# Kernel optimization log

Hardware: AMD Instinct MI355X
Metric: run time of the kernel (lower is better)

Reference implementation:

```python
import jax, jax.numpy as jnp
import numpy as np

# Qwen3-0.6B-like config; 4 equal-length requests flattened into [R*S, H]
L, R, S, H = 2, 4, 1024, 1024
NH, NKV, DH = 16, 8, 128
FF = 3072
EPS = 1e-6
THETA = 1e6
SCALE = 0.02  # weight init scale to keep activations sane


def setup_inputs() -> dict:
    key = jax.random.key(0)
    ks = jax.random.split(key, 8)
    return {
        "hidden_states": jax.random.normal(ks[0], (R * S, H), jnp.float32),
        "Wq": jax.random.normal(ks[1], (L, H, NH * DH), jnp.float32) * SCALE,
        "Wk": jax.random.normal(ks[2], (L, H, NKV * DH), jnp.float32) * SCALE,
        "Wv": jax.random.normal(ks[3], (L, H, NKV * DH), jnp.float32) * SCALE,
        "Wo": jax.random.normal(ks[4], (L, NH * DH, H), jnp.float32) * SCALE,
        "q_norm_w": jnp.ones((L, DH), jnp.float32),
        "k_norm_w": jnp.ones((L, DH), jnp.float32),
        "ln1_w": jnp.ones((L, H), jnp.float32),
        "ln2_w": jnp.ones((L, H), jnp.float32),
        "Wg": jax.random.normal(ks[5], (L, H, FF), jnp.float32) * SCALE,
        "Wu": jax.random.normal(ks[6], (L, H, FF), jnp.float32) * SCALE,
        "Wd": jax.random.normal(ks[7], (L, FF, H), jnp.float32) * SCALE,
        "final_norm_w": jnp.ones((H,), jnp.float32),
    }


def _rms(x, w):
    return x * jax.lax.rsqrt(jnp.mean(x * x, axis=-1, keepdims=True) + EPS) * w


def _rope_tables():
    inv_freq = 1.0 / (THETA ** (jnp.arange(0, DH, 2, dtype=jnp.float32) / DH))
    pos = jnp.arange(S, dtype=jnp.float32)  # per-request positions 0..S-1 (prefill)
    freqs = pos[:, None] * inv_freq[None, :]        # [S, DH/2]
    emb = jnp.concatenate([freqs, freqs], axis=-1)  # [S, DH]
    return jnp.cos(emb), jnp.sin(emb)


def _rotate_half(x):
    x1, x2 = jnp.split(x, 2, axis=-1)
    return jnp.concatenate([-x2, x1], axis=-1)


def _apply_rope(x, cos, sin):
    # x: [R, heads, S, DH]; cos/sin: [S, DH]
    c = cos[None, None]
    s = sin[None, None]
    return x * c + _rotate_half(x) * s


def reference(hidden_states, Wq, Wk, Wv, Wo, q_norm_w, k_norm_w, ln1_w, ln2_w,
              Wg, Wu, Wd, final_norm_w):
    cos, sin = _rope_tables()
    causal = jnp.tril(jnp.ones((S, S), dtype=bool))  # per-request causal mask
    neg = jnp.finfo(hidden_states.dtype).min
    scaling = 1.0 / jnp.sqrt(jnp.asarray(DH, hidden_states.dtype))

    x = hidden_states
    for l in range(L):
        # --- attention block ---
        residual = x
        h = _rms(x, ln1_w[l])                       # [R*S, H]
        q = (h @ Wq[l]).reshape(R, S, NH, DH)
        k = (h @ Wk[l]).reshape(R, S, NKV, DH)
        v = (h @ Wv[l]).reshape(R, S, NKV, DH)
        q = _rms(q, q_norm_w[l]).transpose(0, 2, 1, 3)   # [R, NH, S, DH]
        k = _rms(k, k_norm_w[l]).transpose(0, 2, 1, 3)   # [R, NKV, S, DH]
        v = v.transpose(0, 2, 1, 3)                      # [R, NKV, S, DH]
        q = _apply_rope(q, cos, sin)
        k = _apply_rope(k, cos, sin)
        # GQA: repeat KV heads
        rep = NH // NKV
        k = jnp.repeat(k, rep, axis=1)
        v = jnp.repeat(v, rep, axis=1)
        scores = jnp.einsum('rhqd,rhkd->rhqk', q, k) * scaling
        scores = jnp.where(causal[None, None], scores, neg)
        attn = jax.nn.softmax(scores, axis=-1)
        o = jnp.einsum('rhqk,rhkd->rhqd', attn, v)       # [R, NH, S, DH]
        o = o.transpose(0, 2, 1, 3).reshape(R * S, NH * DH)
        x = residual + o @ Wo[l]
        # --- MLP block ---
        residual = x
        h = _rms(x, ln2_w[l])
        x = residual + (jax.nn.silu(h @ Wg[l]) * (h @ Wu[l])) @ Wd[l]
    return _rms(x, final_norm_w)
```

## Files before the change

### kernel.cpp

```cpp
#include <hip/hip_runtime.h>
#include <hip/hip_bf16.h>

typedef __bf16 bf16;
typedef __bf16 bf16x8 __attribute__((ext_vector_type(8)));
typedef float f32x4 __attribute__((ext_vector_type(4)));

#define DEVINL __device__ __forceinline__

constexpr int L_ = 2, R_ = 4, S_ = 1024, H_ = 1024;
constexpr int NH_ = 16, NKV_ = 8, DH_ = 128;
constexpr int FF_ = 3072;
constexpr int T_ = R_ * S_;

DEVINL void gload16(const bf16* g, bf16* l) {
    __builtin_amdgcn_global_load_lds(
        (const __attribute__((address_space(1))) void*)g,
        (__attribute__((address_space(3))) void*)l, 16, 0, 0);
}

__global__ void rope_tables_kernel(float* __restrict__ cosb, float* __restrict__ sinb) {
    int s = blockIdx.x;
    int i = threadIdx.x;
    float inv = __expf(-(float)i * (1.0f / 64.0f) * 13.815510557964274f);
    float f = (float)s * inv;
    cosb[s * 64 + i] = cosf(f);
    sinb[s * 64 + i] = sinf(f);
}

template <bool OUT_BF16>
__global__ __launch_bounds__(256) void rmsnorm_kernel(const float* __restrict__ x,
                                                      const float* __restrict__ w,
                                                      void* __restrict__ out) {
    int row = blockIdx.x;
    const float* xr = x + (size_t)row * H_;
    int t = threadIdx.x;
    float v[4];
    float ss = 0.f;
#pragma unroll
    for (int j = 0; j < 4; ++j) {
        v[j] = xr[t + 256 * j];
        ss += v[j] * v[j];
    }
#pragma unroll
    for (int off = 32; off; off >>= 1) ss += __shfl_xor(ss, off);
    __shared__ float part[4];
    if ((t & 63) == 0) part[t >> 6] = ss;
    __syncthreads();
    ss = part[0] + part[1] + part[2] + part[3];
    float r = rsqrtf(ss * (1.0f / (float)H_) + 1e-6f);
#pragma unroll
    for (int j = 0; j < 4; ++j) {
        int c = t + 256 * j;
        float o = v[j] * r * w[c];
        if constexpr (OUT_BF16)
            ((bf16*)out)[(size_t)row * H_ + c] = (bf16)o;
        else
            ((float*)out)[(size_t)row * H_ + c] = o;
    }
}

__global__ __launch_bounds__(256) void transpose_all_kernel(
    const float* __restrict__ Wq, const float* __restrict__ Wk, const float* __restrict__ Wv,
    const float* __restrict__ Wo, const float* __restrict__ Wg, const float* __restrict__ Wu,
    const float* __restrict__ Wd, bf16* __restrict__ wqkv_t, bf16* __restrict__ wo_t,
    bf16* __restrict__ wgu_t, bf16* __restrict__ wd_t) {
    __shared__ float tile[32][33];
    int bid = blockIdx.x;
    const float* in;
    bf16* out;
    int Rk, Cn, mode, tid;
    if (bid < 2048) { in = Wq; out = wqkv_t; Rk = 1024; Cn = 2048; mode = 0; tid = bid; }
    else if (bid < 3072) { in = Wk; out = wqkv_t + (size_t)2048 * 1024; Rk = 1024; Cn = 1024; mode = 0; tid = bid - 2048; }
    else if (bid < 4096) { in = Wv; out = wqkv_t + (size_t)3072 * 1024; Rk = 1024; Cn = 1024; mode = 0; tid = bid - 3072; }
    else if (bid < 6144) { in = Wo; out = wo_t; Rk = 2048; Cn = 1024; mode = 0; tid = bid - 4096; }
    else if (bid < 9216) { in = Wg; out = wgu_t; Rk = 1024; Cn = 3072; mode = 1; tid = bid - 6144; }
    else if (bid < 12288) { in = Wu; out = wgu_t; Rk = 1024; Cn = 3072; mode = 2; tid = bid - 9216; }
    else { in = Wd; out = wd_t; Rk = 3072; Cn = 1024; mode = 0; tid = bid - 12288; }
    int nbx = Cn >> 5;
    int c0 = (tid % nbx) * 32, r0 = (tid / nbx) * 32;
    int t = threadIdx.x;
    int tc = t & 31, tr = t >> 5;
#pragma unroll
    for (int i = 0; i < 4; ++i) {
        int r = tr + i * 8;
        tile[r][tc] = in[(size_t)(r0 + r) * Cn + c0 + tc];
    }
    __syncthreads();
#pragma unroll
    for (int i = 0; i < 4; ++i) {
        int c = c0 + tr + i * 8;
        int n = (mode == 0) ? c : (((c >> 4) << 5) + ((mode == 2) ? 16 : 0) + (c & 15));
        out[(size_t)n * Rk + r0 + tc] = (bf16)tile[tc][tr + i * 8];
    }
}

__global__ __launch_bounds__(256) void vt_kernel(const bf16* __restrict__ qkv,
                                                 bf16* __restrict__ vt) {
    __shared__ bf16 tile[32][34];
    int s0 = blockIdx.x * 32, c0 = blockIdx.y * 32, r = blockIdx.z;
    int t = threadIdx.x, tc = t & 31, tr = t >> 5;
#pragma unroll
    for (int i = 0; i < 4; ++i) {
        int s = tr + i * 8;
        tile[s][tc] = qkv[(size_t)(r * 1024 + s0 + s) * 4096 + 3072 + c0 + tc];
    }
    __syncthreads();
#pragma unroll
    for (int i = 0; i < 4; ++i) {
        int c = tr + i * 8;
        vt[((size_t)(r * 1024 + c0 + c)) * 1024 + s0 + tc] = tile[tc][c];
    }
}

template <int EPI>
__global__ __launch_bounds__(512, 4) void gemmP_kernel(const bf16* __restrict__ A,
                                                       const bf16* __restrict__ Bt,
                                                       void* __restrict__ out,
                                                       int M, int N, int K) {
    __shared__ bf16 lds[36864];
    const int NT = K >> 5;
    int nbm = M >> 7, nbn = N >> 8;
    int slice = nbn >> 3;
    int id = blockIdx.x;
    int xcd = id & 7, wi = id >> 3;
    int bm = (wi / slice) << 7;
    int bn = (xcd * slice + wi % slice) << 8;
    int t = threadIdx.x, lane = t & 63, w = t >> 6;
    int wm = w >> 2, wn = w & 3;
    int hi = lane >> 4, f = lane & 15;

    int srow = t >> 2;
    int ssc = (t & 3) ^ ((srow >> 1) & 3);
    const bf16* aSrc = A + (size_t)(bm + srow) * K + (ssc << 3);
    const bf16* b0Src = Bt + (size_t)(bn + srow) * K + (ssc << 3);
    const bf16* b1Src = Bt + (size_t)(bn + 128 + srow) * K + (ssc << 3);

    f32x4 acc[4][4] = {};

    auto stage = [&](int tt, int sb) {
        gload16(aSrc + tt * 32, lds + sb * 4096 + w * 512);
        gload16(b0Src + tt * 32, lds + 12288 + sb * 8192 + w * 512);
        gload16(b1Src + tt * 32, lds + 12288 + sb * 8192 + 4096 + w * 512);
    };

    stage(0, 0);
    stage(1, 1);
    asm volatile("s_waitcnt vmcnt(3)" ::: "memory");
    __builtin_amdgcn_s_barrier();

    int cb = 0;
    for (int tau = 0; tau < NT; ++tau) {
        const bf16* aB = lds + cb * 4096;
        const bf16* bB = lds + 12288 + cb * 8192;
        if (tau + 2 < NT) stage(tau + 2, (cb == 0) ? 2 : cb - 1);
        bf16x8 af[4], bfv[4];
#pragma unroll
        for (int mf = 0; mf < 4; ++mf) {
            int row = wm * 64 + mf * 16 + f;
            af[mf] = *(const bf16x8*)(aB + row * 32 + ((hi ^ ((row >> 1) & 3)) << 3));
        }
#pragma unroll
        for (int nf = 0; nf < 4; ++nf) {
            int row = wn * 64 + nf * 16 + f;
            bfv[nf] = *(const bf16x8*)(bB + row * 32 + ((hi ^ ((row >> 1) & 3)) << 3));
        }
        __builtin_amdgcn_s_setprio(1);
#pragma unroll
        for (int mf = 0; mf < 4; ++mf)
#pragma unroll
            for (int nf = 0; nf < 4; ++nf)
                acc[mf][nf] = __builtin_amdgcn_mfma_f32_16x16x32_bf16(af[mf], bfv[nf],
                                                                      acc[mf][nf], 0, 0, 0);
        __builtin_amdgcn_s_setprio(0);
        if (tau < NT - 2)
            asm volatile("s_waitcnt vmcnt(3)" ::: "memory");
        else
            asm volatile("s_waitcnt vmcnt(0)" ::: "memory");
        __builtin_amdgcn_s_barrier();
        cb = (cb == 2) ? 0 : cb + 1;
    }

    int rb = bm + wm * 64 + hi * 4;
#pragma unroll
    for (int mf = 0; mf < 4; ++mf) {
        if constexpr (EPI == 5) {
#pragma unroll
            for (int p = 0; p < 2; ++p) {
                int col = ((bn + wn * 64) >> 1) + p * 16 + f;
#pragma unroll
                for (int g = 0; g < 4; ++g) {
                    float gv = acc[mf][2 * p][g], uv = acc[mf][2 * p + 1][g];
                    float sv = gv / (1.0f + __expf(-gv));
                    ((bf16*)out)[(size_t)(rb + mf * 16 + g) * (N / 2) + col] = (bf16)(sv * uv);
                }
            }
        } else {
            int cb2 = bn + wn * 64 + f;
#pragma unroll
            for (int nf = 0; nf < 4; ++nf)
#pragma unroll
                for (int g = 0; g < 4; ++g)
                    ((bf16*)out)[(size_t)(rb + mf * 16 + g) * N + cb2 + nf * 16] =
                        (bf16)acc[mf][nf][g];
        }
    }
}

template <int EPI>
__global__ __launch_bounds__(256, 2) void gemmD_kernel(const bf16* __restrict__ A,
                                                       const bf16* __restrict__ Bt,
                                                       void* __restrict__ out,
                                                       const float* __restrict__ res,
                                                       int M, int N, int K) {
    __shared__ bf16 lds[36864];
    const int NT = K >> 6;
    int nbm = M >> 6;
    int id = blockIdx.x;
    int xcd = id & 7, wi = id >> 3;
    int bm = (wi % nbm) << 6, bn = xcd << 7;
    int t = threadIdx.x, lane = t & 63, w = t >> 6;
    int wm = w >> 1, wn = w & 1;
    int hi = lane >> 4, f = lane & 15;

    int ar0 = t >> 3, ac0 = t & 7;
    const bf16* aS0 = A + (size_t)(bm + ar0) * K + (((ac0 ^ (ar0 & 7)) & 7) << 3);
    const bf16* aS1 = A + (size_t)(bm + 32 + ar0) * K + (((ac0 ^ ((ar0 + 32) & 7)) & 7) << 3);
    const bf16* bS[4];
#pragma unroll
    for (int j = 0; j < 4; ++j) {
        int row = j * 32 + ar0;
        bS[j] = Bt + (size_t)(bn + row) * K + (((ac0 ^ (row & 7)) & 7) << 3);
    }

    f32x4 acc[2][4] = {};

    auto stage = [&](int tt, int sb) {
        gload16(aS0 + tt * 64, lds + sb * 4096 + w * 512);
        gload16(aS1 + tt * 64, lds + sb * 4096 + 2048 + w * 512);
#pragma unroll
        for (int j = 0; j < 4; ++j)
            gload16(bS[j] + tt * 64, lds + 12288 + sb * 8192 + j * 2048 + w * 512);
    };

    stage(0, 0);
    stage(1, 1);
    asm volatile("s_waitcnt vmcnt(6)" ::: "memory");
    __builtin_amdgcn_s_barrier();

    int cb = 0;
    for (int tau = 0; tau < NT; ++tau) {
        const bf16* aB = lds + cb * 4096;
        const bf16* bB = lds + 12288 + cb * 8192;
        if (tau + 2 < NT) stage(tau + 2, (cb == 0) ? 2 : cb - 1);
        bf16x8 af[2][2], bfv[2][4];
#pragma unroll
        for (int kh = 0; kh < 2; ++kh) {
            int q = kh * 4 + hi;
#pragma unroll
            for (int mf = 0; mf < 2; ++mf) {
                int row = wm * 32 + mf * 16 + f;
                af[kh][mf] = *(const bf16x8*)(aB + row * 64 + ((q ^ (row & 7)) << 3));
            }
#pragma unroll
            for (int nf = 0; nf < 4; ++nf) {
                int row = wn * 64 + nf * 16 + f;
                bfv[kh][nf] = *(const bf16x8*)(bB + row * 64 + ((q ^ (row & 7)) << 3));
            }
        }
        __builtin_amdgcn_s_setprio(1);
#pragma unroll
        for (int kh = 0; kh < 2; ++kh)
#pragma unroll
            for (int mf = 0; mf < 2; ++mf)
#pragma unroll
                for (int nf = 0; nf < 4; ++nf)
                    acc[mf][nf] = __builtin_amdgcn_mfma_f32_16x16x32_bf16(
                        af[kh][mf], bfv[kh][nf], acc[mf][nf], 0, 0, 0);
        __builtin_amdgcn_s_setprio(0);
        if (tau < NT - 2)
            asm volatile("s_waitcnt vmcnt(6)" ::: "memory");
        else
            asm volatile("s_waitcnt vmcnt(0)" ::: "memory");
        __builtin_amdgcn_s_barrier();
        cb = (cb == 2) ? 0 : cb + 1;
    }

    int rb = bm + wm * 32 + hi * 4;
    int cb2 = bn + wn * 64 + f;
#pragma unroll
    for (int mf = 0; mf < 2; ++mf)
#pragma unroll
        for (int nf = 0; nf < 4; ++nf)
#pragma unroll
            for (int g = 0; g < 4; ++g) {
                size_t idx = (size_t)(rb + mf * 16 + g) * N + cb2 + nf * 16;
                ((float*)out)[idx] = acc[mf][nf][g] + res[idx];
            }
}

DEVINL void head_norm_rope(const bf16* __restrict__ src, const float* __restrict__ w,
                           const float* __restrict__ cosb, const float* __restrict__ sinb,
                           int s, int ln, bf16* __restrict__ dst) {
    float x0 = (float)src[ln], x1 = (float)src[ln + 32];
    float x2 = (float)src[ln + 64], x3 = (float)src[ln + 96];
    float ss = x0 * x0 + x1 * x1 + x2 * x2 + x3 * x3;
#pragma unroll
    for (int off = 16; off; off >>= 1) ss += __shfl_xor(ss, off);
    float rr = rsqrtf(ss * (1.0f / 128.0f) + 1e-6f);
    float n0 = x0 * rr * w[ln], n1 = x1 * rr * w[ln + 32];
    float n2 = x2 * rr * w[ln + 64], n3 = x3 * rr * w[ln + 96];
    float c0 = cosb[s * 64 + ln], c1 = cosb[s * 64 + ln + 32];
    float s0 = sinb[s * 64 + ln], s1 = sinb[s * 64 + ln + 32];
    dst[ln] = (bf16)(n0 * c0 - n2 * s0);
    dst[ln + 32] = (bf16)(n1 * c1 - n3 * s1);
    dst[ln + 64] = (bf16)(n2 * c0 + n0 * s0);
    dst[ln + 96] = (bf16)(n3 * c1 + n1 * s1);
}

__global__ __launch_bounds__(256) void qkv_post_kernel(const bf16* __restrict__ qkv,
                                                       const float* __restrict__ qw,
                                                       const float* __restrict__ kw,
                                                       const float* __restrict__ cosb,
                                                       const float* __restrict__ sinb,
                                                       bf16* __restrict__ qo,
                                                       bf16* __restrict__ ko) {
    int tok = blockIdx.x;
    int r = tok >> 10, s = tok & 1023;
    int t = threadIdx.x;
    int g = t >> 5;
    int ln = t & 31;
    const bf16* row = qkv + (size_t)tok * 4096;
#pragma unroll
    for (int hh = 0; hh < 2; ++hh) {
        int h = g + hh * 8;
        head_norm_rope(row + h * 128, qw, cosb, sinb, s, ln,
                       qo + ((size_t)(r * NH_ + h) * S_ + s) * 128);
    }
    head_norm_rope(row + 2048 + g * 128, kw, cosb, sinb, s, ln,
                   ko + ((size_t)(r * NKV_ + g) * S_ + s) * 128);
}

__global__ __launch_bounds__(256, 2) void flash_kernel(const bf16* __restrict__ q,
                                                       const bf16* __restrict__ k,
                                                       const bf16* __restrict__ vt,
                                                       bf16* __restrict__ out) {
    __shared__ bf16 Kl[64 * 128];
    __shared__ bf16 Vl[128 * 64];
    __shared__ bf16 Pl[4][32 * 64];
    int bid = blockIdx.x;
    int grp = bid & 63, slot = bid >> 6;
    int strip = (slot < 4) ? (7 - slot) : (slot - 4);
    int h = 2 * (grp & 7) + ((grp >> 3) & 1);
    int r = grp >> 4;
    int kvh = h >> 1;

    int t = threadIdx.x, lane = t & 63, w = t >> 6;
    int arow = lane & 15, hi = lane >> 4;
    int a7 = arow & 7;
    int grow = hi * 4;
    int qbase = strip * 128 + w * 32;

    const bf16* qp = q + ((size_t)(r * NH_ + h) * S_ + qbase) * 128;
    bf16x8 qf[2][4];
#pragma unroll
    for (int m = 0; m < 2; ++m)
#pragma unroll
        for (int kc = 0; kc < 4; ++kc)
            qf[m][kc] = *(const bf16x8*)(qp + (size_t)(m * 16 + arow) * 128 + kc * 32 + hi * 8);

    const bf16* kp = k + (size_t)(r * NKV_ + kvh) * S_ * 128;
    const bf16* vp = vt + (size_t)(r * NKV_ + kvh) * 128 * S_;

    int krow0 = t >> 4, kc16 = t & 15;
    int vrow0 = t >> 3, vc16 = t & 7;

    bf16x8 ones;
#pragma unroll
    for (int i = 0; i < 8; ++i) ones[i] = (bf16)1.0f;

    f32x4 ao[2][8] = {};
    f32x4 aol[2] = {};
    const float scale = 0.08838834764831845f;

    int nt = 2 * (strip + 1);
    bf16x8 krs[4], vrs[4];
#pragma unroll
    for (int i = 0; i < 4; ++i)
        krs[i] = *(const bf16x8*)(kp + (size_t)(krow0 + 16 * i) * 128 + kc16 * 8);
#pragma unroll
    for (int i = 0; i < 4; ++i)
        vrs[i] = *(const bf16x8*)(vp + (size_t)(vrow0 + 32 * i) * S_ + vc16 * 8);

    for (int it = 0; it < nt; ++it) {
        int kv0 = it * 64;
        __syncthreads();
#pragma unroll
        for (int i = 0; i < 4; ++i) {
            int row = krow0 + 16 * i;
            *(bf16x8*)(&Kl[row * 128 + ((kc16 ^ (row & 7)) * 8)]) = krs[i];
        }
#pragma unroll
        for (int i = 0; i < 4; ++i) {
            int row = vrow0 + 32 * i;
            *(bf16x8*)(&Vl[row * 64 + ((vc16 ^ (row & 7)) * 8)]) = vrs[i];
        }
        __syncthreads();
        if (it + 1 < nt) {
            int kvn = kv0 + 64;
#pragma unroll
            for (int i = 0; i < 4; ++i)
                krs[i] = *(const bf16x8*)(kp + (size_t)(kvn + krow0 + 16 * i) * 128 + kc16 * 8);
#pragma unroll
            for (int i = 0; i < 4; ++i)
                vrs[i] = *(const bf16x8*)(vp + (size_t)(vrow0 + 32 * i) * S_ + kvn + vc16 * 8);
        }
        f32x4 sc[2][4];
#pragma unroll
        for (int m = 0; m < 2; ++m)
#pragma unroll
            for (int n = 0; n < 4; ++n) sc[m][n] = (f32x4){0.f, 0.f, 0.f, 0.f};
#pragma unroll
        for (int n = 0; n < 4; ++n) {
            int krw = n * 16 + arow;
#pragma unroll
            for (int kc = 0; kc < 4; ++kc) {
                bf16x8 kf = *(const bf16x8*)(&Kl[krw * 128 + (((kc * 4 + hi) ^ a7) * 8)]);
                sc[0][n] = __builtin_amdgcn_mfma_f32_16x16x32_bf16(qf[0][kc], kf, sc[0][n], 0, 0, 0);
                sc[1][n] = __builtin_amdgcn_mfma_f32_16x16x32_bf16(qf[1][kc], kf, sc[1][n], 0, 0, 0);
            }
        }
#pragma unroll
        for (int m = 0; m < 2; ++m) {
            bool msk = (kv0 + 64 > qbase + m * 16);
#pragma unroll
            for (int n = 0; n < 4; ++n) {
                int chnk = 2 * n + (arow >> 3);
#pragma unroll
                for (int g = 0; g < 4; ++g) {
                    float sval = sc[m][n][g] * scale;
                    if (msk && (kv0 + n * 16 + arow > qbase + m * 16 + grow + g)) sval = -1e30f;
                    float p = __expf(sval);
                    int qr = m * 16 + grow + g;
                    Pl[w][qr * 64 + ((chnk ^ (qr & 7)) * 8) + a7] = (bf16)p;
                }
            }
        }
        bf16x8 pf[2][2];
#pragma unroll
        for (int m = 0; m < 2; ++m) {
            int qr = m * 16 + arow;
#pragma unroll
            for (int ks = 0; ks < 2; ++ks)
                pf[m][ks] = *(const bf16x8*)(&Pl[w][qr * 64 + (((ks * 4 + hi) ^ a7) * 8)]);
        }
#pragma unroll
        for (int m = 0; m < 2; ++m) {
            aol[m] = __builtin_amdgcn_mfma_f32_16x16x32_bf16(pf[m][0], ones, aol[m], 0, 0, 0);
            aol[m] = __builtin_amdgcn_mfma_f32_16x16x32_bf16(pf[m][1], ones, aol[m], 0, 0, 0);
        }
#pragma unroll
        for (int c = 0; c < 8; ++c) {
            int vrw = c * 16 + arow;
#pragma unroll
            for (int ks = 0; ks < 2; ++ks) {
                bf16x8 vf = *(const bf16x8*)(&Vl[vrw * 64 + (((ks * 4 + hi) ^ a7) * 8)]);
                ao[0][c] = __builtin_amdgcn_mfma_f32_16x16x32_bf16(pf[0][ks], vf, ao[0][c], 0, 0, 0);
                ao[1][c] = __builtin_amdgcn_mfma_f32_16x16x32_bf16(pf[1][ks], vf, ao[1][c], 0, 0, 0);
            }
        }
    }
#pragma unroll
    for (int m = 0; m < 2; ++m) {
        f32x4 rl;
#pragma unroll
        for (int g = 0; g < 4; ++g) rl[g] = 1.0f / aol[m][g];
#pragma unroll
        for (int c = 0; c < 8; ++c)
#pragma unroll
            for (int g = 0; g < 4; ++g) {
                int rq = qbase + m * 16 + grow + g;
                out[(size_t)(r * S_ + rq) * 2048 + h * 128 + c * 16 + arow] =
                    (bf16)(ao[m][c][g] * rl[g]);
            }
    }
}

extern "C" void kernel_launch(void* const* d_in, const int* in_sizes, int n_in,
                              void* d_out, int out_size, void* d_ws, size_t ws_size,
                              hipStream_t stream) {
    const float* hidden = (const float*)d_in[0];
    const float* Wq = (const float*)d_in[1];
    const float* Wk = (const float*)d_in[2];
    const float* Wv = (const float*)d_in[3];
    const float* Wo = (const float*)d_in[4];
    const float* qnw = (const float*)d_in[5];
    const float* knw = (const float*)d_in[6];
    const float* ln1 = (const float*)d_in[7];
    const float* ln2 = (const float*)d_in[8];
    const float* Wg = (const float*)d_in[9];
    const float* Wu = (const float*)d_in[10];
    const float* Wd = (const float*)d_in[11];
    const float* fnw = (const float*)d_in[12];
    float* out = (float*)d_out;

    char* ws = (char*)d_ws;
    size_t off = 0;
    auto alloc = [&](size_t bytes) -> char* {
        char* p = ws + off;
        off += (bytes + 255) & ~(size_t)255;
        return p;
    };
    float* cosb = (float*)alloc((size_t)S_ * 64 * 4);
    float* sinb = (float*)alloc((size_t)S_ * 64 * 4);
    float* x_ws = (float*)alloc((size_t)T_ * H_ * 4);
    bf16* hbuf = (bf16*)alloc((size_t)T_ * H_ * 2);
    bf16* qkv = (bf16*)alloc((size_t)T_ * 4096 * 2);
    bf16* act = qkv;
    bf16* qb = (bf16*)alloc((size_t)R_ * NH_ * S_ * 128 * 2);
    bf16* kb = (bf16*)alloc((size_t)R_ * NKV_ * S_ * 128 * 2);
    bf16* vtb = (bf16*)alloc((size_t)R_ * NKV_ * 128 * S_ * 2);
    bf16* attn = (bf16*)alloc((size_t)T_ * 2048 * 2);
    bf16* wqkv_t = (bf16*)alloc((size_t)4096 * 1024 * 2);
    bf16* wo_t = (bf16*)alloc((size_t)1024 * 2048 * 2);
    bf16* wgu_t = (bf16*)alloc((size_t)6144 * 1024 * 2);
    bf16* wd_t = (bf16*)alloc((size_t)1024 * 3072 * 2);

    rope_tables_kernel<<<S_, 64, 0, stream>>>(cosb, sinb);

    const float* xin = hidden;
    for (int l = 0; l < L_; ++l) {
        transpose_all_kernel<<<15360, 256, 0, stream>>>(
            Wq + (size_t)l * H_ * 2048, Wk + (size_t)l * H_ * 1024, Wv + (size_t)l * H_ * 1024,
            Wo + (size_t)l * 2048 * 1024, Wg + (size_t)l * H_ * 3072, Wu + (size_t)l * H_ * 3072,
            Wd + (size_t)l * 3072 * 1024, wqkv_t, wo_t, wgu_t, wd_t);

        rmsnorm_kernel<true><<<T_, 256, 0, stream>>>(xin, ln1 + (size_t)l * H_, hbuf);
        gemmP_kernel<1><<<512, 512, 0, stream>>>(hbuf, wqkv_t, qkv, 4096, 4096, 1024);
        qkv_post_kernel<<<T_, 256, 0, stream>>>(qkv, qnw + (size_t)l * 128, knw + (size_t)l * 128,
                                                cosb, sinb, qb, kb);
        vt_kernel<<<dim3(32, 32, 4), 256, 0, stream>>>(qkv, vtb);
        flash_kernel<<<512, 256, 0, stream>>>(qb, kb, vtb, attn);
        gemmD_kernel<4><<<512, 256, 0, stream>>>(attn, wo_t, x_ws, xin, 4096, 1024, 2048);
        rmsnorm_kernel<true><<<T_, 256, 0, stream>>>(x_ws, ln2 + (size_t)l * H_, hbuf);
        gemmP_kernel<5><<<768, 512, 0, stream>>>(hbuf, wgu_t, act, 4096, 6144, 1024);
        gemmD_kernel<4><<<512, 256, 0, stream>>>(act, wd_t, x_ws, x_ws, 4096, 1024, 3072);
        xin = x_ws;
    }
    rmsnorm_kernel<false><<<T_, 256, 0, stream>>>(x_ws, fnw, out);
}
```

Before: 513.6 us.

## Use 256x256-tile triple-buffered GEMM for QKV projection and vectorize RMSNorm loads

```diff
diff --git a/kernel.cpp b/kernel.cpp
--- a/kernel.cpp
+++ b/kernel.cpp
@@ -34,13 +34,8 @@
     int row = blockIdx.x;
     const float* xr = x + (size_t)row * H_;
     int t = threadIdx.x;
-    float v[4];
-    float ss = 0.f;
-#pragma unroll
-    for (int j = 0; j < 4; ++j) {
-        v[j] = xr[t + 256 * j];
-        ss += v[j] * v[j];
-    }
+    f32x4 v = *(const f32x4*)(xr + t * 4);
+    float ss = v[0] * v[0] + v[1] * v[1] + v[2] * v[2] + v[3] * v[3];
 #pragma unroll
     for (int off = 32; off; off >>= 1) ss += __shfl_xor(ss, off);
     __shared__ float part[4];
@@ -48,14 +43,14 @@
     __syncthreads();
     ss = part[0] + part[1] + part[2] + part[3];
     float r = rsqrtf(ss * (1.0f / (float)H_) + 1e-6f);
+    f32x4 wv = *(const f32x4*)(w + t * 4);
 #pragma unroll
     for (int j = 0; j < 4; ++j) {
-        int c = t + 256 * j;
-        float o = v[j] * r * w[c];
+        float o = v[j] * r * wv[j];
         if constexpr (OUT_BF16)
-            ((bf16*)out)[(size_t)row * H_ + c] = (bf16)o;
+            ((bf16*)out)[(size_t)row * H_ + t * 4 + j] = (bf16)o;
         else
-            ((float*)out)[(size_t)row * H_ + c] = o;
+            ((float*)out)[(size_t)row * H_ + t * 4 + j] = o;
     }
 }
 
@@ -113,6 +108,88 @@
 }
 
 template <int EPI>
+__global__ __launch_bounds__(512, 2) void gemmT_kernel(const bf16* __restrict__ A,
+                                                       const bf16* __restrict__ Bt,
+                                                       void* __restrict__ out,
+                                                       int M, int N, int K) {
+    __shared__ bf16 lds[49152];
+    const int NT = K >> 5;
+    int nbm = M >> 8, nbn = N >> 8;
+    int slice = nbn >> 3;
+    int id = blockIdx.x;
+    int xcd = id & 7, wi = id >> 3;
+    int bm = (wi / slice) << 8;
+    int bn = (xcd * slice + wi % slice) << 8;
+    int t = threadIdx.x, lane = t & 63, w = t >> 6;
+    int wm = w >> 2, wn = w & 3;
+    int hi = lane >> 4, f = lane & 15;
+
+    int r0 = t >> 2;
+    int so = (((t & 3) ^ ((r0 >> 1) & 3)) << 3);
+    const bf16* aS0 = A + (size_t)(bm + r0) * K + so;
+    const bf16* aS1 = A + (size_t)(bm + 128 + r0) * K + so;
+    const bf16* bS0 = Bt + (size_t)(bn + r0) * K + so;
+    const bf16* bS1 = Bt + (size_t)(bn + 128 + r0) * K + so;
+
+    f32x4 acc[8][4] = {};
+
+    auto stage = [&](int tt, int sb) {
+        gload16(aS0 + tt * 32, lds + sb * 8192 + w * 512);
+        gload16(aS1 + tt * 32, lds + sb * 8192 + 4096 + w * 512);
+        gload16(bS0 + tt * 32, lds + 24576 + sb * 8192 + w * 512);
+        gload16(bS1 + tt * 32, lds + 24576 + sb * 8192 + 4096 + w * 512);
+    };
+
+    stage(0, 0);
+    stage(1, 1);
+    asm volatile("s_waitcnt vmcnt(4)" ::: "memory");
+    __builtin_amdgcn_s_barrier();
+
+    int cb = 0;
+    for (int tau = 0; tau < NT; ++tau) {
+        const bf16* aB = lds + cb * 8192;
+        const bf16* bB = lds + 24576 + cb * 8192;
+        if (tau + 2 < NT) stage(tau + 2, (cb == 0) ? 2 : cb - 1);
+        bf16x8 af[8], bfv[4];
+#pragma unroll
+        for (int mf = 0; mf < 8; ++mf) {
+            int row = wm * 128 + mf * 16 + f;
+            af[mf] = *(const bf16x8*)(aB + row * 32 + ((hi ^ ((row >> 1) & 3)) << 3));
+        }
+#pragma unroll
+        for (int nf = 0; nf < 4; ++nf) {
+            int row = wn * 64 + nf * 16 + f;
+            bfv[nf] = *(const bf16x8*)(bB + row * 32 + ((hi ^ ((row >> 1) & 3)) << 3));
+        }
+        __builtin_amdgcn_s_setprio(1);
+#pragma unroll
+        for (int mf = 0; mf < 8; ++mf)
+#pragma unroll
+            for (int nf = 0; nf < 4; ++nf)
+                acc[mf][nf] = __builtin_amdgcn_mfma_f32_16x16x32_bf16(af[mf], bfv[nf],
+                                                                      acc[mf][nf], 0, 0, 0);
+        __builtin_amdgcn_s_setprio(0);
+        if (tau < NT - 2)
+            asm volatile("s_waitcnt vmcnt(4)" ::: "memory");
+        else
+            asm volatile("s_waitcnt vmcnt(0)" ::: "memory");
+        __builtin_amdgcn_s_barrier();
+        cb = (cb == 2) ? 0 : cb + 1;
+    }
+
+    int rb = bm + wm * 128 + hi * 4;
+    int cb2 = bn + wn * 64 + f;
+#pragma unroll
+    for (int mf = 0; mf < 8; ++mf)
+#pragma unroll
+        for (int nf = 0; nf < 4; ++nf)
+#pragma unroll
+            for (int g = 0; g < 4; ++g)
+                ((bf16*)out)[(size_t)(rb + mf * 16 + g) * N + cb2 + nf * 16] =
+                    (bf16)acc[mf][nf][g];
+}
+
+template <int EPI>
 __global__ __launch_bounds__(512, 4) void gemmP_kernel(const bf16* __restrict__ A,
                                                        const bf16* __restrict__ Bt,
                                                        void* __restrict__ out,
@@ -535,7 +612,7 @@
             Wd + (size_t)l * 3072 * 1024, wqkv_t, wo_t, wgu_t, wd_t);
 
         rmsnorm_kernel<true><<<T_, 256, 0, stream>>>(xin, ln1 + (size_t)l * H_, hbuf);
-        gemmP_kernel<1><<<512, 512, 0, stream>>>(hbuf, wqkv_t, qkv, 4096, 4096, 1024);
+        gemmT_kernel<1><<<256, 512, 0, stream>>>(hbuf, wqkv_t, qkv, 4096, 4096, 1024);
         qkv_post_kernel<<<T_, 256, 0, stream>>>(qkv, qnw + (size_t)l * 128, knw + (size_t)l * 128,
                                                 cosb, sinb, qb, kb);
         vt_kernel<<<dim3(32, 32, 4), 256, 0, stream>>>(qkv, vtb);
```

After: 508.8 us (median of 3 runs). About the same (-0.9%).
